# Optimization experiments

Hardware: AMD Instinct MI355X
Metric: run time of the kernel (lower is better)

Reference implementation:

```python
import jax, jax.numpy as jnp
import numpy as np

N_NODES = 100000


def gcn_conv(x, src, dst, W, b, n_nodes):
    # PyG GCNConv: x' = D^{-1/2} (A + I) D^{-1/2} (x @ W) + b
    # src/dst already include self-loops.
    h = x @ W  # [N, out]
    deg = jax.ops.segment_sum(jnp.ones_like(src, dtype=x.dtype), dst,
                              num_segments=n_nodes)  # includes self-loops -> deg >= 1
    dinv = jax.lax.rsqrt(deg)
    norm = dinv[src] * dinv[dst]  # [E+N]
    msgs = h[src] * norm[:, None]  # [E+N, out]
    out = jax.ops.segment_sum(msgs, dst, num_segments=n_nodes)
    return out + b


def setup_inputs() -> dict:
    key = jax.random.key(0)
    k1, k2, k3, k4 = jax.random.split(key, 4)
    in_dim, hid_dim, out_dim = 64, 128, 64
    n_edges = 1_600_000
    x = jax.random.normal(k1, (N_NODES, in_dim), dtype=jnp.float32)
    edge_index = jax.random.randint(k2, (2, n_edges), 0, N_NODES, dtype=jnp.int64)
    # Glorot-ish init for weights
    W1 = jax.random.normal(k3, (in_dim, hid_dim), dtype=jnp.float32) * (1.0 / np.sqrt(in_dim))
    W2 = jax.random.normal(k4, (hid_dim, out_dim), dtype=jnp.float32) * (1.0 / np.sqrt(hid_dim))
    b1 = jnp.zeros((hid_dim,), dtype=jnp.float32)
    b2 = jnp.zeros((out_dim,), dtype=jnp.float32)
    return {"x": x, "edge_index": edge_index, "W1": W1, "b1": b1, "W2": W2, "b2": b2}


def reference(x, edge_index, W1, b1, W2, b2):
    n = x.shape[0]
    loops = jnp.arange(n, dtype=edge_index.dtype)
    src = jnp.concatenate([edge_index[0], loops])
    dst = jnp.concatenate([edge_index[1], loops])
    h = gcn_conv(x, src, dst, W1, b1, n)
    h = jax.nn.relu(h)
    out = gcn_conv(h, src, dst, W2, b2, n)
    return out
```

## Files before the change

### kernel.cpp

```cpp
#include <hip/hip_runtime.h>
#include <hip/hip_fp16.h>


#define DIM 64
#define NB 256
#define SPAN 391
#define BK_TILE 4096
#define BK_PER 16

typedef _Float16 f16x8 __attribute__((ext_vector_type(8)));
typedef float f32x4 __attribute__((ext_vector_type(4)));

__device__ __forceinline__ void atomAddF(float* p, float v) {
    unsafeAtomicAdd(p, v);
}

__device__ __forceinline__ void h8_add(const float4 v, float* acc) {
    const __half2* hp = (const __half2*)&v;
    #pragma unroll
    for (int i = 0; i < 4; ++i) {
        float2 t = __half22float2(hp[i]);
        acc[2 * i] += t.x;
        acc[2 * i + 1] += t.y;
    }
}
__device__ __forceinline__ float4 f8_to_h8(const float* f) {
    __half2 hh[4];
    hh[0] = __float22half2_rn(make_float2(f[0], f[1]));
    hh[1] = __float22half2_rn(make_float2(f[2], f[3]));
    hh[2] = __float22half2_rn(make_float2(f[4], f[5]));
    hh[3] = __float22half2_rn(make_float2(f[6], f[7]));
    return *(float4*)hh;
}

__global__ __launch_bounds__(256) void k_zero256(int* p) {
    p[threadIdx.x] = 0;
}
__global__ __launch_bounds__(256) void k_hist256(const int* __restrict__ ei,
                                                 int* __restrict__ bucketCnt, int E) {
    __shared__ int h[NB];
    const int tid = threadIdx.x;
    h[tid] = 0;
    __syncthreads();
    const int base = blockIdx.x * BK_TILE;
    #pragma unroll
    for (int j = 0; j < BK_TILE; j += 256) {
        int e = base + j + tid;
        if (e < E) atomicAdd(&h[(unsigned)ei[E + e] / (unsigned)SPAN], 1);
    }
    __syncthreads();
    if (h[tid]) atomicAdd(&bucketCnt[tid], h[tid]);
}
__global__ __launch_bounds__(256) void k_scan_b(const int* __restrict__ bucketCnt,
                                                int* __restrict__ bucketBase,
                                                int* __restrict__ gcur) {
    __shared__ int s[NB];
    const int tid = threadIdx.x;
    int v = bucketCnt[tid];
    s[tid] = v;
    __syncthreads();
    for (int off = 1; off < NB; off <<= 1) {
        int t = (tid >= off) ? s[tid - off] : 0;
        __syncthreads();
        s[tid] += t;
        __syncthreads();
    }
    int ex = s[tid] - v;
    bucketBase[tid] = ex;
    gcur[tid] = ex;
    if (tid == NB - 1) bucketBase[NB] = s[NB - 1];
}

__global__ __launch_bounds__(256) void k_bucket(const int* __restrict__ ei,
                                                int* __restrict__ gcur,
                                                unsigned* __restrict__ pairs, int E) {
    __shared__ int scn[NB];
    __shared__ int run[NB];
    __shared__ int lbase[NB];
    __shared__ int gbase[NB];
    __shared__ unsigned stage[BK_TILE];
    __shared__ unsigned char bkt[BK_TILE];
    const int tid = threadIdx.x;
    const int base = blockIdx.x * BK_TILE;

    scn[tid] = 0;
    __syncthreads();

    unsigned pv[BK_PER];
    int bv[BK_PER];
    #pragma unroll
    for (int j = 0; j < BK_PER; ++j) {
        int e = base + j * 256 + tid;
        if (e < E) {
            unsigned s = (unsigned)ei[e];
            unsigned d = (unsigned)ei[E + e];
            int b = (int)(d / (unsigned)SPAN);
            bv[j] = b;
            pv[j] = (s << 9) | (d - (unsigned)b * SPAN);
            atomicAdd(&scn[b], 1);
        } else bv[j] = -1;
    }
    __syncthreads();
    int c = scn[tid];
    for (int off = 1; off < 256; off <<= 1) {
        int t = (tid >= off) ? scn[tid - off] : 0;
        __syncthreads();
        scn[tid] += t;
        __syncthreads();
    }
    int ex = scn[tid] - c;
    lbase[tid] = ex;
    run[tid] = ex;
    if (c > 0) gbase[tid] = atomicAdd(&gcur[tid], c);
    __syncthreads();

    #pragma unroll
    for (int j = 0; j < BK_PER; ++j) {
        if (bv[j] >= 0) {
            int p = atomicAdd(&run[bv[j]], 1);
            stage[p] = pv[j];
            bkt[p] = (unsigned char)bv[j];
        }
    }
    __syncthreads();

    int total = min(BK_TILE, E - base);
    for (int i = tid; i < total; i += 256) {
        int bb = bkt[i];
        pairs[gbase[bb] + (i - lbase[bb])] = stage[i];
    }
}

__global__ __launch_bounds__(256) void k_finish(const unsigned* __restrict__ pairs,
                                                const int* __restrict__ bucketBase,
                                                int* __restrict__ row_ptr,
                                                float* __restrict__ dinv,
                                                int* __restrict__ col, int N) {
    __shared__ int lh[512];
    __shared__ int sa[512];
    __shared__ int sb[512];
    __shared__ int lcur[SPAN];
    const int tid = threadIdx.x;
    const int b = blockIdx.x;
    const int lo = b * SPAN;
    const int hi = min(lo + SPAN, N);
    const int nn = hi - lo;
    const int p0 = bucketBase[b];
    const int p1 = bucketBase[b + 1];

    for (int i = tid; i < 512; i += 256) lh[i] = 0;
    __syncthreads();
    for (int e = p0 + tid; e < p1; e += 256)
        atomicAdd(&lh[pairs[e] & 511u], 1);
    __syncthreads();
    int* cur = sa;
    int* nxt = sb;
    for (int i = tid; i < 512; i += 256) sa[i] = lh[i];
    __syncthreads();
    for (int off = 1; off < 512; off <<= 1) {
        for (int i = tid; i < 512; i += 256)
            nxt[i] = cur[i] + ((i >= off) ? cur[i - off] : 0);
        __syncthreads();
        int* t = cur; cur = nxt; nxt = t;
    }
    for (int i = tid; i < nn; i += 256) {
        int cnt  = lh[i];
        int base = p0 + cur[i] - cnt;
        row_ptr[lo + i] = base;
        lcur[i] = base;
        dinv[lo + i] = rsqrtf(1.0f + (float)cnt);
    }
    if (b == NB - 1 && tid == 0) row_ptr[N] = p1;
    __syncthreads();
    for (int e = p0 + tid; e < p1; e += 256) {
        unsigned pr = pairs[e];
        int pos = atomicAdd(&lcur[pr & 511u], 1);
        col[pos] = (int)(pr >> 9);
    }
}

__global__ __launch_bounds__(256) void k_prescale_h(const float* __restrict__ x,
                                                    const float* __restrict__ dinv,
                                                    __half* __restrict__ Y, int n) {
    int g = blockIdx.x * 256 + threadIdx.x;
    int i = g >> 3, seg = g & 7;
    if (i >= n) return;
    float di = dinv[i];
    float4 a = ((const float4*)x)[(long)i * 16 + seg * 2];
    float4 b = ((const float4*)x)[(long)i * 16 + seg * 2 + 1];
    float f[8] = {a.x * di, a.y * di, a.z * di, a.w * di,
                  b.x * di, b.y * di, b.z * di, b.w * di};
    ((float4*)Y)[(long)i * 8 + seg] = f8_to_h8(f);
}

template<bool BIAS, bool OUT_HALF>
__global__ __launch_bounds__(256) void k_agg_h(const int* __restrict__ row_ptr,
                                               const int* __restrict__ col,
                                               const float* __restrict__ dinv,
                                               const __half* __restrict__ ph,
                                               const float* __restrict__ bias,
                                               void* __restrict__ outv, int n) {
    int g = blockIdx.x * 32 + (threadIdx.x >> 3);
    if (g >= n) return;
    int lane = threadIdx.x & 7;
    const float4* h4 = (const float4*)ph;
    float accA[8] = {}, accB[8] = {};
    h8_add(h4[(long)g * 8 + lane], accA);
    int e = row_ptr[g], e1 = row_ptr[g + 1];
    for (; e + 8 <= e1; e += 8) {
        int s0 = col[e], s1 = col[e + 1], s2 = col[e + 2], s3 = col[e + 3];
        int s4 = col[e + 4], s5 = col[e + 5], s6 = col[e + 6], s7 = col[e + 7];
        float4 v0 = h4[(long)s0 * 8 + lane];
        float4 v1 = h4[(long)s1 * 8 + lane];
        float4 v2 = h4[(long)s2 * 8 + lane];
        float4 v3 = h4[(long)s3 * 8 + lane];
        float4 v4 = h4[(long)s4 * 8 + lane];
        float4 v5 = h4[(long)s5 * 8 + lane];
        float4 v6 = h4[(long)s6 * 8 + lane];
        float4 v7 = h4[(long)s7 * 8 + lane];
        h8_add(v0, accA); h8_add(v1, accB);
        h8_add(v2, accA); h8_add(v3, accB);
        h8_add(v4, accA); h8_add(v5, accB);
        h8_add(v6, accA); h8_add(v7, accB);
    }
    for (; e + 2 <= e1; e += 2) {
        float4 v0 = h4[(long)col[e] * 8 + lane];
        float4 v1 = h4[(long)col[e + 1] * 8 + lane];
        h8_add(v0, accA); h8_add(v1, accB);
    }
    if (e < e1) h8_add(h4[(long)col[e] * 8 + lane], accA);

    float di = dinv[g];
    float r[8];
    #pragma unroll
    for (int i = 0; i < 8; ++i) r[i] = (accA[i] + accB[i]) * di;
    if (OUT_HALF) {
        ((float4*)outv)[(long)g * 8 + lane] = f8_to_h8(r);
    } else {
        if (BIAS) {
            float4 b0 = ((const float4*)bias)[lane * 2];
            float4 b1 = ((const float4*)bias)[lane * 2 + 1];
            r[0] += b0.x; r[1] += b0.y; r[2] += b0.z; r[3] += b0.w;
            r[4] += b1.x; r[5] += b1.y; r[6] += b1.z; r[7] += b1.w;
        }
        ((float4*)outv)[(long)g * 16 + lane * 2]     = make_float4(r[0], r[1], r[2], r[3]);
        ((float4*)outv)[(long)g * 16 + lane * 2 + 1] = make_float4(r[4], r[5], r[6], r[7]);
    }
}

__global__ __launch_bounds__(256) void k_wconv(const float* __restrict__ W1,
                                               const float* __restrict__ W2,
                                               _Float16* __restrict__ W1t,
                                               _Float16* __restrict__ W2t) {
    int idx = blockIdx.x * 256 + threadIdx.x;
    if (idx < 8192) {
        int n = idx >> 6, k = idx & 63;
        W1t[idx] = (_Float16)W1[k * 128 + n];
    } else if (idx < 16384) {
        int j = idx - 8192;
        int n = j >> 7, k = j & 127;
        W2t[j] = (_Float16)W2[k * 64 + n];
    }
}

__global__ __launch_bounds__(256) void k_mlp_mfma(const _Float16* __restrict__ G,
                                                  const _Float16* __restrict__ W1t,
                                                  const float* __restrict__ b1,
                                                  const _Float16* __restrict__ W2t,
                                                  const float* __restrict__ dscale,
                                                  _Float16* __restrict__ T,
                                                  int M) {
    __shared__ _Float16 Hs[64 * 136];
    __shared__ _Float16 Os[64 * 72];
    const int tid = threadIdx.x;
    const int row0 = blockIdx.x * 64;
    const int wv = tid >> 6;
    const int lane = tid & 63;
    const int lr = lane & 15;
    const int lg = lane >> 4;

    const int arow = row0 + wv * 16 + lr;
    f16x8 a0 = {}, a1 = {};
    if (arow < M) {
        a0 = *(const f16x8*)(G + (long)arow * 64 + lg * 8);
        a1 = *(const f16x8*)(G + (long)arow * 64 + 32 + lg * 8);
    }
    const _Float16* wb1 = W1t + lr * 64 + lg * 8;
    f32x4 acc[8];
    #pragma unroll
    for (int nt = 0; nt < 8; ++nt) acc[nt] = (f32x4){0.f, 0.f, 0.f, 0.f};
    #pragma unroll
    for (int nt = 0; nt < 8; ++nt) {
        f16x8 b0 = *(const f16x8*)(wb1 + nt * 1024);
        f16x8 bK = *(const f16x8*)(wb1 + nt * 1024 + 32);
        acc[nt] = __builtin_amdgcn_mfma_f32_16x16x32_f16(a0, b0, acc[nt], 0, 0, 0);
        acc[nt] = __builtin_amdgcn_mfma_f32_16x16x32_f16(a1, bK, acc[nt], 0, 0, 0);
    }
    #pragma unroll
    for (int nt = 0; nt < 8; ++nt) {
        float bv = b1[nt * 16 + lr];
        #pragma unroll
        for (int r = 0; r < 4; ++r) {
            float h = fmaxf(acc[nt][r] + bv, 0.f);
            Hs[(wv * 16 + lg * 4 + r) * 136 + nt * 16 + lr] = (_Float16)h;
        }
    }
    __syncthreads();

    const _Float16* wb2 = W2t + lr * 128 + lg * 8;
    const _Float16* hrow = Hs + (wv * 16 + lr) * 136 + lg * 8;
    f32x4 acc2[4];
    #pragma unroll
    for (int nt = 0; nt < 4; ++nt) acc2[nt] = (f32x4){0.f, 0.f, 0.f, 0.f};
    #pragma unroll
    for (int kk = 0; kk < 4; ++kk) {
        f16x8 a = *(const f16x8*)(hrow + kk * 32);
        #pragma unroll
        for (int nt = 0; nt < 4; ++nt) {
            f16x8 b = *(const f16x8*)(wb2 + nt * 2048 + kk * 32);
            acc2[nt] = __builtin_amdgcn_mfma_f32_16x16x32_f16(a, b, acc2[nt], 0, 0, 0);
        }
    }
    float sc[4];
    #pragma unroll
    for (int r = 0; r < 4; ++r) {
        int gr = row0 + wv * 16 + lg * 4 + r;
        sc[r] = (gr < M) ? dscale[gr] : 0.f;
    }
    #pragma unroll
    for (int nt = 0; nt < 4; ++nt) {
        #pragma unroll
        for (int r = 0; r < 4; ++r)
            Os[(wv * 16 + lg * 4 + r) * 72 + nt * 16 + lr] = (_Float16)(acc2[nt][r] * sc[r]);
    }
    __syncthreads();

    {
        int r = tid >> 2, c0 = (tid & 3) * 16;
        int gr = row0 + r;
        if (gr < M) {
            f16x8 v0 = *(const f16x8*)(Os + r * 72 + c0);
            f16x8 v1 = *(const f16x8*)(Os + r * 72 + c0 + 8);
            *(f16x8*)(T + (long)gr * 64 + c0) = v0;
            *(f16x8*)(T + (long)gr * 64 + c0 + 8) = v1;
        }
    }
}

__global__ __launch_bounds__(256) void k_init_deg(float* deg, int n) {
    int i = blockIdx.x * 256 + threadIdx.x;
    if (i < n) deg[i] = 1.0f;
}
__global__ __launch_bounds__(256) void k_count_deg(const int* __restrict__ ei, float* deg, int E) {
    int e = blockIdx.x * 256 + threadIdx.x;
    if (e < E) atomAddF(&deg[ei[E + e]], 1.0f);
}
__global__ __launch_bounds__(256) void k_rsqrt(float* deg, int n) {
    int i = blockIdx.x * 256 + threadIdx.x;
    if (i < n) deg[i] = rsqrtf(deg[i]);
}
template<bool BIAS>
__global__ __launch_bounds__(256) void k_self(const float* __restrict__ src,
                                              const float* __restrict__ dinv,
                                              const float* __restrict__ b,
                                              float* __restrict__ out, int n) {
    int g = blockIdx.x * 256 + threadIdx.x;
    int i = g >> 4, c = g & 15;
    if (i >= n) return;
    float di = dinv[i];
    float s = di * di;
    float4 v = *(const float4*)&src[(long)i * DIM + c * 4];
    float4 r = make_float4(v.x * s, v.y * s, v.z * s, v.w * s);
    if (BIAS) {
        float4 bv = *(const float4*)&b[c * 4];
        r.x += bv.x; r.y += bv.y; r.z += bv.z; r.w += bv.w;
    }
    *(float4*)&out[(long)i * DIM + c * 4] = r;
}
__global__ __launch_bounds__(256) void k_edge_agg(const int* __restrict__ ei,
                                                  const float* __restrict__ dinv,
                                                  const float* __restrict__ h,
                                                  float* __restrict__ out, int E) {
    int t = threadIdx.x;
    int e = blockIdx.x * 16 + (t >> 4);
    if (e >= E) return;
    int lane = t & 15;
    int s = ei[e];
    int d = ei[E + e];
    float norm = dinv[s] * dinv[d];
    float4 hv = *(const float4*)&h[(long)s * DIM + lane * 4];
    float* o = &out[(long)d * DIM + lane * 4];
    atomAddF(o + 0, hv.x * norm);
    atomAddF(o + 1, hv.y * norm);
    atomAddF(o + 2, hv.z * norm);
    atomAddF(o + 3, hv.w * norm);
}
__global__ __launch_bounds__(256) void k_mlp_f(const float* __restrict__ G,
                                               const float* __restrict__ W1,
                                               const float* __restrict__ b1,
                                               const float* __restrict__ W2,
                                               float* __restrict__ T, int M) {
    __shared__ float Ws[64 * 128];
    __shared__ float HA[64 * 132];
    const int tid = threadIdx.x;
    const int row0 = blockIdx.x * 64;
    const int ty = tid >> 4;
    const int tx = tid & 15;
    #pragma unroll
    for (int l = 0; l < 4; ++l) {
        int idx = l * 256 + tid;
        int r = idx >> 4, cv = idx & 15;
        int gr = row0 + r;
        float4 v = make_float4(0.f, 0.f, 0.f, 0.f);
        if (gr < M) v = *(const float4*)&G[(long)gr * DIM + cv * 4];
        *(float4*)&HA[r * 68 + cv * 4] = v;
    }
    #pragma unroll
    for (int l = 0; l < 8; ++l) {
        int idx = (l * 256 + tid) * 4;
        *(float4*)&Ws[idx] = *(const float4*)&W1[idx];
    }
    __syncthreads();
    float4 accA[4], accB[4];
    #pragma unroll
    for (int i = 0; i < 4; ++i) {
        accA[i] = make_float4(0.f, 0.f, 0.f, 0.f);
        accB[i] = make_float4(0.f, 0.f, 0.f, 0.f);
    }
    for (int k4 = 0; k4 < 64; k4 += 4) {
        float4 a[4];
        #pragma unroll
        for (int i = 0; i < 4; ++i) a[i] = *(const float4*)&HA[(ty * 4 + i) * 68 + k4];
        #pragma unroll
        for (int kk = 0; kk < 4; ++kk) {
            const float* wr = &Ws[(k4 + kk) * 128 + tx * 8];
            float4 wA = *(const float4*)wr;
            float4 wB = *(const float4*)(wr + 4);
            #pragma unroll
            for (int i = 0; i < 4; ++i) {
                float ak = (&a[i].x)[kk];
                accA[i].x += ak * wA.x; accA[i].y += ak * wA.y;
                accA[i].z += ak * wA.z; accA[i].w += ak * wA.w;
                accB[i].x += ak * wB.x; accB[i].y += ak * wB.y;
                accB[i].z += ak * wB.z; accB[i].w += ak * wB.w;
            }
        }
    }
    __syncthreads();
    {
        float4 bA = *(const float4*)&b1[tx * 8];
        float4 bB = *(const float4*)&b1[tx * 8 + 4];
        #pragma unroll
        for (int i = 0; i < 4; ++i) {
            float4 hA = make_float4(fmaxf(accA[i].x + bA.x, 0.f), fmaxf(accA[i].y + bA.y, 0.f),
                                    fmaxf(accA[i].z + bA.z, 0.f), fmaxf(accA[i].w + bA.w, 0.f));
            float4 hB = make_float4(fmaxf(accB[i].x + bB.x, 0.f), fmaxf(accB[i].y + bB.y, 0.f),
                                    fmaxf(accB[i].z + bB.z, 0.f), fmaxf(accB[i].w + bB.w, 0.f));
            *(float4*)&HA[(ty * 4 + i) * 132 + tx * 8 + 0] = hA;
            *(float4*)&HA[(ty * 4 + i) * 132 + tx * 8 + 4] = hB;
        }
    }
    #pragma unroll
    for (int l = 0; l < 8; ++l) {
        int idx = (l * 256 + tid) * 4;
        *(float4*)&Ws[idx] = *(const float4*)&W2[idx];
    }
    __syncthreads();
    float4 o[4];
    #pragma unroll
    for (int i = 0; i < 4; ++i) o[i] = make_float4(0.f, 0.f, 0.f, 0.f);
    for (int k4 = 0; k4 < 128; k4 += 4) {
        float4 a[4];
        #pragma unroll
        for (int i = 0; i < 4; ++i) a[i] = *(const float4*)&HA[(ty * 4 + i) * 132 + k4];
        #pragma unroll
        for (int kk = 0; kk < 4; ++kk) {
            float4 w = *(const float4*)&Ws[(k4 + kk) * 64 + tx * 4];
            #pragma unroll
            for (int i = 0; i < 4; ++i) {
                float ak = (&a[i].x)[kk];
                o[i].x += ak * w.x; o[i].y += ak * w.y;
                o[i].z += ak * w.z; o[i].w += ak * w.w;
            }
        }
    }
    #pragma unroll
    for (int i = 0; i < 4; ++i) {
        int gr = row0 + ty * 4 + i;
        if (gr < M) *(float4*)&T[(long)gr * DIM + tx * 4] = o[i];
    }
}

extern "C" void kernel_launch(void* const* d_in, const int* in_sizes, int n_in,
                              void* d_out, int out_size, void* d_ws, size_t ws_size,
                              hipStream_t stream) {
    const float* x  = (const float*)d_in[0];
    const int*   ei = (const int*)d_in[1];
    const float* W1 = (const float*)d_in[2];
    const float* b1 = (const float*)d_in[3];
    const float* W2 = (const float*)d_in[4];
    const float* b2 = (const float*)d_in[5];
    float* out = (float*)d_out;

    const int N = in_sizes[0] / DIM;
    const int E = in_sizes[1] / 2;

    const int gn   = (N + 255) / 256;
    const int ge   = (E + 255) / 256;
    const int gagg = (N + 31) / 32;
    const int gmlp = (N + 63) / 64;
    const int grow8 = ((long)N * 8 + 255) / 256;
    const int gbk  = (E + BK_TILE - 1) / BK_TILE;

    size_t off = 0;
    auto bump = [&](size_t bytes) { size_t o = off; off = (off + bytes + 255) & ~(size_t)255; return o; };
    size_t o_dinv   = bump((size_t)N * 4);
    size_t o_rowptr = bump((size_t)(N + 1) * 4);
    size_t o_bcnt   = bump(NB * 4);
    size_t o_bbase  = bump((NB + 1) * 4);
    size_t o_gcur   = bump(NB * 4);
    size_t o_col    = bump((size_t)E * 4);
    size_t o_X      = bump((size_t)N * DIM * 2);
    size_t o_Y      = bump((size_t)N * DIM * 2);
    size_t o_W1t    = bump(128 * 64 * 2);
    size_t o_W2t    = bump(64 * 128 * 2);
    size_t need_csr = off;

    char* ws = (char*)d_ws;

    if (ws_size >= need_csr) {
        float*    dinv   = (float*)(ws + o_dinv);
        int*      rowptr = (int*)(ws + o_rowptr);
        int*      bcnt   = (int*)(ws + o_bcnt);
        int*      bbase  = (int*)(ws + o_bbase);
        int*      gcur   = (int*)(ws + o_gcur);
        int*      col    = (int*)(ws + o_col);
        __half*   X      = (__half*)(ws + o_X);
        __half*   Y      = (__half*)(ws + o_Y);
        unsigned* pairs  = (unsigned*)(ws + o_Y);
        _Float16* W1t    = (_Float16*)(ws + o_W1t);
        _Float16* W2t    = (_Float16*)(ws + o_W2t);

        k_wconv<<<64, 256, 0, stream>>>(W1, W2, W1t, W2t);
        k_zero256<<<1, 256, 0, stream>>>(bcnt);
        k_hist256<<<gbk, 256, 0, stream>>>(ei, bcnt, E);
        k_scan_b<<<1, 256, 0, stream>>>(bcnt, bbase, gcur);
        k_bucket<<<gbk, 256, 0, stream>>>(ei, gcur, pairs, E);
        k_finish<<<NB, 256, 0, stream>>>(pairs, bbase, rowptr, dinv, col, N);

        k_prescale_h<<<grow8, 256, 0, stream>>>(x, dinv, Y, N);
        k_agg_h<false, true><<<gagg, 256, 0, stream>>>(rowptr, col, dinv, Y, nullptr, X, N);
        k_mlp_mfma<<<gmlp, 256, 0, stream>>>((const _Float16*)X, W1t, b1, W2t, dinv,
                                             (_Float16*)X, N);
        k_agg_h<true, false><<<gagg, 256, 0, stream>>>(rowptr, col, dinv, X, b2, out, N);
    } else {
        float* dinv = (float*)ws;
        float* buf  = (float*)(ws + 512 * 1024);
        int grow16 = ((long)N * 16 + 255) / 256;
        int gedge = (E + 15) / 16;

        k_init_deg<<<gn, 256, 0, stream>>>(dinv, N);
        k_count_deg<<<ge, 256, 0, stream>>>(ei, dinv, E);
        k_rsqrt<<<gn, 256, 0, stream>>>(dinv, N);

        k_self<false><<<grow16, 256, 0, stream>>>(x, dinv, nullptr, buf, N);
        k_edge_agg<<<gedge, 256, 0, stream>>>(ei, dinv, x, buf, E);
        k_mlp_f<<<gmlp, 256, 0, stream>>>(buf, W1, b1, W2, buf, N);
        k_self<true><<<grow16, 256, 0, stream>>>(buf, dinv, b2, out, N);
        k_edge_agg<<<gedge, 256, 0, stream>>>(ei, dinv, buf, out, E);
    }
}
```

Before: 239.1 us.

## Fuse prescale into CSR finish, aggregation into MLP, zeroing into weight conversion

Folds the bucket-count zeroing into the weight-conversion kernel, moves the dinv prescale of x into k_finish so each bucket block scales its own rows, and merges the first-layer aggregation with the MFMA MLP so aggregated rows stay in shared memory instead of going through global memory. The pairs buffer gets its own workspace region because Y is now written while pairs is still being read. This removes three launches and one global round trip of the intermediate features. In exchange the MLP kernel now runs a gather-heavy phase with 64 rows per block, which may lower occupancy and latency hiding, and k_finish does extra work on only 256 blocks.

Measured after the change: 236.3 us. Within noise of the previous version (-1.2%).

```diff
diff --git a/kernel.cpp b/kernel.cpp
--- a/kernel.cpp
+++ b/kernel.cpp
@@ -33,9 +33,23 @@
     return *(float4*)hh;
 }
 
-__global__ __launch_bounds__(256) void k_zero256(int* p) {
-    p[threadIdx.x] = 0;
-}
+__global__ __launch_bounds__(256) void k_wconv(const float* __restrict__ W1,
+                                               const float* __restrict__ W2,
+                                               _Float16* __restrict__ W1t,
+                                               _Float16* __restrict__ W2t,
+                                               int* __restrict__ bcnt) {
+    int idx = blockIdx.x * 256 + threadIdx.x;
+    if (blockIdx.x == 0) bcnt[threadIdx.x] = 0;
+    if (idx < 8192) {
+        int n = idx >> 6, k = idx & 63;
+        W1t[idx] = (_Float16)W1[k * 128 + n];
+    } else if (idx < 16384) {
+        int j = idx - 8192;
+        int n = j >> 7, k = j & 127;
+        W2t[j] = (_Float16)W2[k * 64 + n];
+    }
+}
+
 __global__ __launch_bounds__(256) void k_hist256(const int* __restrict__ ei,
                                                  int* __restrict__ bucketCnt, int E) {
     __shared__ int h[NB];
@@ -135,7 +149,9 @@
                                                 const int* __restrict__ bucketBase,
                                                 int* __restrict__ row_ptr,
                                                 float* __restrict__ dinv,
-                                                int* __restrict__ col, int N) {
+                                                int* __restrict__ col,
+                                                const float* __restrict__ x,
+                                                __half* __restrict__ Y, int N) {
     __shared__ int lh[512];
     __shared__ int sa[512];
     __shared__ int sb[512];
@@ -177,20 +193,16 @@
         int pos = atomicAdd(&lcur[pr & 511u], 1);
         col[pos] = (int)(pr >> 9);
     }
-}
-
-__global__ __launch_bounds__(256) void k_prescale_h(const float* __restrict__ x,
-                                                    const float* __restrict__ dinv,
-                                                    __half* __restrict__ Y, int n) {
-    int g = blockIdx.x * 256 + threadIdx.x;
-    int i = g >> 3, seg = g & 7;
-    if (i >= n) return;
-    float di = dinv[i];
-    float4 a = ((const float4*)x)[(long)i * 16 + seg * 2];
-    float4 b = ((const float4*)x)[(long)i * 16 + seg * 2 + 1];
-    float f[8] = {a.x * di, a.y * di, a.z * di, a.w * di,
-                  b.x * di, b.y * di, b.z * di, b.w * di};
-    ((float4*)Y)[(long)i * 8 + seg] = f8_to_h8(f);
+    const int seg = tid & 7;
+    for (int rr = tid >> 3; rr < nn; rr += 32) {
+        float di = rsqrtf(1.0f + (float)lh[rr]);
+        long row = lo + rr;
+        float4 a = ((const float4*)x)[row * 16 + seg * 2];
+        float4 c = ((const float4*)x)[row * 16 + seg * 2 + 1];
+        float f[8] = {a.x * di, a.y * di, a.z * di, a.w * di,
+                      c.x * di, c.y * di, c.z * di, c.w * di};
+        ((float4*)Y)[row * 8 + seg] = f8_to_h8(f);
+    }
 }
 
 template<bool BIAS, bool OUT_HALF>
@@ -248,43 +260,69 @@
     }
 }
 
-__global__ __launch_bounds__(256) void k_wconv(const float* __restrict__ W1,
-                                               const float* __restrict__ W2,
-                                               _Float16* __restrict__ W1t,
-                                               _Float16* __restrict__ W2t) {
-    int idx = blockIdx.x * 256 + threadIdx.x;
-    if (idx < 8192) {
-        int n = idx >> 6, k = idx & 63;
-        W1t[idx] = (_Float16)W1[k * 128 + n];
-    } else if (idx < 16384) {
-        int j = idx - 8192;
-        int n = j >> 7, k = j & 127;
-        W2t[j] = (_Float16)W2[k * 64 + n];
-    }
-}
-
-__global__ __launch_bounds__(256) void k_mlp_mfma(const _Float16* __restrict__ G,
-                                                  const _Float16* __restrict__ W1t,
-                                                  const float* __restrict__ b1,
-                                                  const _Float16* __restrict__ W2t,
-                                                  const float* __restrict__ dscale,
-                                                  _Float16* __restrict__ T,
-                                                  int M) {
-    __shared__ _Float16 Hs[64 * 136];
-    __shared__ _Float16 Os[64 * 72];
+__global__ __launch_bounds__(256) void k_agg_mlp(const int* __restrict__ row_ptr,
+                                                 const int* __restrict__ col,
+                                                 const float* __restrict__ dinv,
+                                                 const __half* __restrict__ Y,
+                                                 const _Float16* __restrict__ W1t,
+                                                 const float* __restrict__ b1,
+                                                 const _Float16* __restrict__ W2t,
+                                                 _Float16* __restrict__ X,
+                                                 int M) {
+    __shared__ __align__(16) _Float16 Xs[64 * 72];
+    __shared__ __align__(16) _Float16 Hs[64 * 136];
     const int tid = threadIdx.x;
     const int row0 = blockIdx.x * 64;
+    const int grp = tid >> 3;
+    const int lane = tid & 7;
+    const float4* h4 = (const float4*)Y;
+
+    #pragma unroll
+    for (int hh = 0; hh < 2; ++hh) {
+        const int lrow = grp + hh * 32;
+        const int g = row0 + lrow;
+        float r[8] = {};
+        if (g < M) {
+            float accA[8] = {}, accB[8] = {};
+            h8_add(h4[(long)g * 8 + lane], accA);
+            int e = row_ptr[g], e1 = row_ptr[g + 1];
+            for (; e + 8 <= e1; e += 8) {
+                int s0 = col[e], s1 = col[e + 1], s2 = col[e + 2], s3 = col[e + 3];
+                int s4 = col[e + 4], s5 = col[e + 5], s6 = col[e + 6], s7 = col[e + 7];
+                float4 v0 = h4[(long)s0 * 8 + lane];
+                float4 v1 = h4[(long)s1 * 8 + lane];
+                float4 v2 = h4[(long)s2 * 8 + lane];
+                float4 v3 = h4[(long)s3 * 8 + lane];
+                float4 v4 = h4[(long)s4 * 8 + lane];
+                float4 v5 = h4[(long)s5 * 8 + lane];
+                float4 v6 = h4[(long)s6 * 8 + lane];
+                float4 v7 = h4[(long)s7 * 8 + lane];
+                h8_add(v0, accA); h8_add(v1, accB);
+                h8_add(v2, accA); h8_add(v3, accB);
+                h8_add(v4, accA); h8_add(v5, accB);
+                h8_add(v6, accA); h8_add(v7, accB);
+            }
+            for (; e + 2 <= e1; e += 2) {
+                float4 v0 = h4[(long)col[e] * 8 + lane];
+                float4 v1 = h4[(long)col[e + 1] * 8 + lane];
+                h8_add(v0, accA); h8_add(v1, accB);
+            }
+            if (e < e1) h8_add(h4[(long)col[e] * 8 + lane], accA);
+            float di = dinv[g];
+            #pragma unroll
+            for (int i = 0; i < 8; ++i) r[i] = (accA[i] + accB[i]) * di;
+        }
+        *(float4*)&Xs[lrow * 72 + lane * 8] = f8_to_h8(r);
+    }
+    __syncthreads();
+
     const int wv = tid >> 6;
-    const int lane = tid & 63;
-    const int lr = lane & 15;
-    const int lg = lane >> 4;
-
-    const int arow = row0 + wv * 16 + lr;
-    f16x8 a0 = {}, a1 = {};
-    if (arow < M) {
-        a0 = *(const f16x8*)(G + (long)arow * 64 + lg * 8);
-        a1 = *(const f16x8*)(G + (long)arow * 64 + 32 + lg * 8);
-    }
+    const int l64 = tid & 63;
+    const int lr = l64 & 15;
+    const int lg = l64 >> 4;
+
+    f16x8 a0 = *(const f16x8*)&Xs[(wv * 16 + lr) * 72 + lg * 8];
+    f16x8 a1 = *(const f16x8*)&Xs[(wv * 16 + lr) * 72 + 32 + lg * 8];
     const _Float16* wb1 = W1t + lr * 64 + lg * 8;
     f32x4 acc[8];
     #pragma unroll
@@ -308,7 +346,7 @@
     __syncthreads();
 
     const _Float16* wb2 = W2t + lr * 128 + lg * 8;
-    const _Float16* hrow = Hs + (wv * 16 + lr) * 136 + lg * 8;
+    const _Float16* hrow = &Hs[(wv * 16 + lr) * 136 + lg * 8];
     f32x4 acc2[4];
     #pragma unroll
     for (int nt = 0; nt < 4; ++nt) acc2[nt] = (f32x4){0.f, 0.f, 0.f, 0.f};
@@ -321,11 +359,12 @@
             acc2[nt] = __builtin_amdgcn_mfma_f32_16x16x32_f16(a, b, acc2[nt], 0, 0, 0);
         }
     }
+    _Float16* Os = Xs;
     float sc[4];
     #pragma unroll
     for (int r = 0; r < 4; ++r) {
         int gr = row0 + wv * 16 + lg * 4 + r;
-        sc[r] = (gr < M) ? dscale[gr] : 0.f;
+        sc[r] = (gr < M) ? dinv[gr] : 0.f;
     }
     #pragma unroll
     for (int nt = 0; nt < 4; ++nt) {
@@ -339,10 +378,10 @@
         int r = tid >> 2, c0 = (tid & 3) * 16;
         int gr = row0 + r;
         if (gr < M) {
-            f16x8 v0 = *(const f16x8*)(Os + r * 72 + c0);
-            f16x8 v1 = *(const f16x8*)(Os + r * 72 + c0 + 8);
-            *(f16x8*)(T + (long)gr * 64 + c0) = v0;
-            *(f16x8*)(T + (long)gr * 64 + c0 + 8) = v1;
+            f16x8 v0 = *(const f16x8*)&Os[r * 72 + c0];
+            f16x8 v1 = *(const f16x8*)&Os[r * 72 + c0 + 8];
+            *(f16x8*)(X + (long)gr * 64 + c0) = v0;
+            *(f16x8*)(X + (long)gr * 64 + c0 + 8) = v1;
         }
     }
 }
@@ -509,7 +548,6 @@
     const int ge   = (E + 255) / 256;
     const int gagg = (N + 31) / 32;
     const int gmlp = (N + 63) / 64;
-    const int grow8 = ((long)N * 8 + 255) / 256;
     const int gbk  = (E + BK_TILE - 1) / BK_TILE;
 
     size_t off = 0;
@@ -522,6 +560,7 @@
     size_t o_col    = bump((size_t)E * 4);
     size_t o_X      = bump((size_t)N * DIM * 2);
     size_t o_Y      = bump((size_t)N * DIM * 2);
+    size_t o_pairs  = bump((size_t)E * 4);
     size_t o_W1t    = bump(128 * 64 * 2);
     size_t o_W2t    = bump(64 * 128 * 2);
     size_t need_csr = off;
@@ -537,21 +576,17 @@
         int*      col    = (int*)(ws + o_col);
         __half*   X      = (__half*)(ws + o_X);
         __half*   Y      = (__half*)(ws + o_Y);
-        unsigned* pairs  = (unsigned*)(ws + o_Y);
+        unsigned* pairs  = (unsigned*)(ws + o_pairs);
         _Float16* W1t    = (_Float16*)(ws + o_W1t);
         _Float16* W2t    = (_Float16*)(ws + o_W2t);
 
-        k_wconv<<<64, 256, 0, stream>>>(W1, W2, W1t, W2t);
-        k_zero256<<<1, 256, 0, stream>>>(bcnt);
+        k_wconv<<<64, 256, 0, stream>>>(W1, W2, W1t, W2t, bcnt);
         k_hist256<<<gbk, 256, 0, stream>>>(ei, bcnt, E);
         k_scan_b<<<1, 256, 0, stream>>>(bcnt, bbase, gcur);
         k_bucket<<<gbk, 256, 0, stream>>>(ei, gcur, pairs, E);
-        k_finish<<<NB, 256, 0, stream>>>(pairs, bbase, rowptr, dinv, col, N);
-
-        k_prescale_h<<<grow8, 256, 0, stream>>>(x, dinv, Y, N);
-        k_agg_h<false, true><<<gagg, 256, 0, stream>>>(rowptr, col, dinv, Y, nullptr, X, N);
-        k_mlp_mfma<<<gmlp, 256, 0, stream>>>((const _Float16*)X, W1t, b1, W2t, dinv,
-                                             (_Float16*)X, N);
+        k_finish<<<NB, 256, 0, stream>>>(pairs, bbase, rowptr, dinv, col, x, Y, N);
+        k_agg_mlp<<<gmlp, 256, 0, stream>>>(rowptr, col, dinv, Y, W1t, b1, W2t,
+                                            (_Float16*)X, N);
         k_agg_h<true, false><<<gagg, 256, 0, stream>>>(rowptr, col, dinv, X, b2, out, N);
     } else {
         float* dinv = (float*)ws;
```
